# Performance work log

Hardware: AMD Instinct MI355X
Metric: run time of the kernel (lower is better)

Reference implementation:

```python
import jax, jax.numpy as jnp
import numpy as np

CHANNELS = 32
HIDDEN = 1024
LAYERS = 8
NODE_TYPES = 7
N_NODES = 500_000
N_EDGES = 2_000_000
NUM_GRAPHS = 1024


def setup_inputs() -> dict:
    key = jax.random.key(0)
    ks = jax.random.split(key, 8)
    nodes = jax.random.randint(ks[0], (N_NODES,), 0, NODE_TYPES)
    sources = jax.random.randint(ks[1], (N_EDGES,), 0, N_NODES)
    targets = jax.random.randint(ks[2], (N_EDGES,), 0, N_NODES)
    # sorted graph ids covering all NUM_GRAPHS graphs (no empty graphs)
    batch = (jnp.arange(N_NODES) * NUM_GRAPHS) // N_NODES
    emb = jax.random.normal(ks[3], (NODE_TYPES, CHANNELS), dtype=jnp.float32)
    # xavier-normal-ish init for the 8 layers x {out, back} 32x32 convs
    xavier_std = (2.0 / (CHANNELS + CHANNELS)) ** 0.5
    conv_w = jax.random.normal(ks[4], (LAYERS, 2, CHANNELS, CHANNELS), dtype=jnp.float32) * xavier_std
    hidden_w = jax.random.normal(ks[5], (CHANNELS, HIDDEN), dtype=jnp.float32) * 0.05
    hidden_b = jax.random.normal(ks[6], (HIDDEN,), dtype=jnp.float32) * 0.05
    out_w = jax.random.normal(ks[7], (HIDDEN, 1), dtype=jnp.float32) * 0.05
    return dict(nodes=nodes, sources=sources, targets=targets, batch=batch,
                emb=emb, conv_w=conv_w, hidden_w=hidden_w, hidden_b=hidden_b,
                out_w=out_w)


def reference(nodes, sources, targets, batch, emb, conv_w, hidden_w, hidden_b, out_w):
    n = nodes.shape[0]
    ones_e = jnp.ones(sources.shape[0], dtype=jnp.float32)
    # norm = 1 / (1 + in-degree), norm_t = 1 / (1 + out-degree)  [N,1]
    norm = (1.0 / (1.0 + jax.ops.segment_sum(ones_e, targets, num_segments=n)))[:, None]
    norm_t = (1.0 / (1.0 + jax.ops.segment_sum(ones_e, sources, num_segments=n)))[:, None]
    node_counts = jax.ops.segment_sum(jnp.ones(n, dtype=jnp.float32), batch,
                                      num_segments=NUM_GRAPHS)

    x = emb[nodes]  # [N, C]

    def conv(x, s, t, nrm, w):
        # x.index_add(0, t, x[s]) -> x + scatter_add of gathered source feats
        agg = nrm * (x + jax.ops.segment_sum(x[s], t, num_segments=n))
        return jax.nn.relu(agg @ w)

    for l in range(LAYERS):
        x = x + conv(x, sources, targets, norm, conv_w[l, 0]) \
              + conv(x, targets, sources, norm_t, conv_w[l, 1])

    # mean pooling per graph
    g = jax.ops.segment_sum(x, batch, num_segments=NUM_GRAPHS) / node_counts[:, None]
    h = jax.nn.relu(g @ hidden_w + hidden_b)
    return (h @ out_w).squeeze(-1)  # [NUM_GRAPHS]
```

## Files before the change

kernel.cpp:

```cpp
#include <hip/hip_runtime.h>

#define CHANNELS 32
#define HIDDEN 1024
#define LAYERS 8
#define NRANGE 8

typedef __attribute__((ext_vector_type(8))) short short8;
typedef __attribute__((ext_vector_type(4))) float float4v;

__device__ __forceinline__ short f2bf_rne(float f) {
    union { float f; unsigned u; } v; v.f = f;
    unsigned r = v.u + 0x7fffu + ((v.u >> 16) & 1u);
    return (short)(r >> 16);
}
__device__ __forceinline__ float bf2f(short h) {
    union { float f; unsigned u; } v; v.u = ((unsigned)(unsigned short)h) << 16;
    return v.f;
}
__device__ __forceinline__ float bfu2f(unsigned short h) {
    union { float f; unsigned u; } v; v.u = ((unsigned)h) << 16;
    return v.f;
}
__device__ __forceinline__ float bflo(unsigned u) {
    union { float f; unsigned u; } v; v.u = u << 16; return v.f;
}
__device__ __forceinline__ float bfhi(unsigned u) {
    union { float f; unsigned u; } v; v.u = u & 0xffff0000u; return v.f;
}
__device__ __forceinline__ unsigned packbf(float x, float y) {
    return ((unsigned)(unsigned short)f2bf_rne(y) << 16) |
            (unsigned)(unsigned short)f2bf_rne(x);
}


__global__ __launch_bounds__(256)
void pre_kernel(const int* __restrict__ src, const int* __restrict__ tgt,
                int* __restrict__ deg2,
                const int* __restrict__ nodes, const float* __restrict__ emb,
                unsigned short* __restrict__ hi0, unsigned short* __restrict__ lo,
                const int* __restrict__ batch, float* __restrict__ counts,
                int n_nodes, int n_edges, int n_graphs, int rsh,
                int degB, int initB) {
    int bid = blockIdx.x;
    int tid = threadIdx.x;
    if (bid < degB) {
        int r = bid & (NRANGE - 1);
        int chunk = bid >> 3;
        int base = chunk * 2048;
#pragma unroll
        for (int j = 0; j < 8; j++) {
            int e = base + j * 256 + tid;
            if (e < n_edges) {
                int t = __builtin_nontemporal_load(tgt + e);
                int s = __builtin_nontemporal_load(src + e);
                if ((t >> rsh) == r) atomicAdd(&deg2[t], 1);
                if ((s >> rsh) == r) atomicAdd(&deg2[n_nodes + s], 1);
            }
        }
    } else if (bid < degB + initB) {
        int gid = (bid - degB) * 256 + tid;
        int i = gid >> 2, c8 = (gid & 3) * 8;
        if (i < n_nodes) {
            const float* e = emb + nodes[i] * CHANNELS + c8;
            short8 hv, lv;
#pragma unroll
            for (int k = 0; k < 8; k++) {
                float v = e[k];
                short hsh = f2bf_rne(v);
                hv[k] = hsh;
                lv[k] = f2bf_rne(v - bf2f(hsh));
            }
            *(short8*)(hi0 + (size_t)i * CHANNELS + c8) = hv;
            *(short8*)(lo  + (size_t)i * CHANNELS + c8) = lv;
        }
    } else {
        int b = (bid - degB - initB) * 256 + tid;
        if (b < n_graphs) {
            int lo_i = 0, hi_i = n_nodes;
            while (lo_i < hi_i) { int mid = (lo_i + hi_i) >> 1; if (batch[mid] < b) lo_i = mid + 1; else hi_i = mid; }
            int s0 = lo_i;
            lo_i = 0; hi_i = n_nodes;
            while (lo_i < hi_i) { int mid = (lo_i + hi_i) >> 1; if (batch[mid] < b + 1) lo_i = mid + 1; else hi_i = mid; }
            counts[b] = (float)(lo_i - s0);
        }
    }
}


__global__ __launch_bounds__(256)
void scan_pass1(const int* __restrict__ deg, int* __restrict__ bs, int n) {
    __shared__ int sh[256];
    int t = threadIdx.x;
    int base = blockIdx.x * 2048 + t * 8;
    int s = 0;
#pragma unroll
    for (int j = 0; j < 8; j++) { int idx = base + j; if (idx < n) s += deg[idx]; }
    sh[t] = s; __syncthreads();
    for (int st = 128; st > 0; st >>= 1) { if (t < st) sh[t] += sh[t + st]; __syncthreads(); }
    if (t == 0) bs[blockIdx.x] = sh[0];
}

__global__ void scan_pass2(int* __restrict__ bs, int nb) {
    __shared__ int sh[1024];
    int t = threadIdx.x;
    int v = (t < nb) ? bs[t] : 0;
    sh[t] = v; __syncthreads();
    for (int off = 1; off < 1024; off <<= 1) {
        int u = (t >= off) ? sh[t - off] : 0; __syncthreads();
        sh[t] += u; __syncthreads();
    }
    if (t < nb) bs[t] = sh[t] - v;
}

__global__ __launch_bounds__(256)
void scan_pass3(const int* __restrict__ deg, const int* __restrict__ bs,
                int* __restrict__ off, int* __restrict__ cur, int n) {
    __shared__ int sh[256];
    int t = threadIdx.x;
    int base = blockIdx.x * 2048 + t * 8;
    int v[8]; int s = 0;
#pragma unroll
    for (int j = 0; j < 8; j++) { int idx = base + j; v[j] = (idx < n) ? deg[idx] : 0; s += v[j]; }
    sh[t] = s; __syncthreads();
    for (int st = 1; st < 256; st <<= 1) {
        int u = (t >= st) ? sh[t - st] : 0; __syncthreads();
        sh[t] += u; __syncthreads();
    }
    int acc = bs[blockIdx.x] + sh[t] - s;
#pragma unroll
    for (int j = 0; j < 8; j++) {
        int idx = base + j;
        if (idx < n) { off[idx] = acc; cur[idx] = acc; }
        acc += v[j];
    }
}


__global__ __launch_bounds__(256)
void scatter_range_kernel(const int* __restrict__ src, const int* __restrict__ tgt,
                          int* __restrict__ cur2, int* __restrict__ nbr,
                          int n_nodes, int n_edges, int rsh, int rbase) {
    int r = rbase + (blockIdx.x & (NRANGE - 1));
    int chunk = blockIdx.x >> 3;
    int base = chunk * 2048;
#pragma unroll
    for (int j = 0; j < 8; j++) {
        int e = base + j * 256 + threadIdx.x;
        if (e < n_edges) {
            int t = __builtin_nontemporal_load(tgt + e);
            int s = __builtin_nontemporal_load(src + e);
            if ((t >> rsh) == r) { int p = atomicAdd(&cur2[t], 1);           nbr[p] = s; }
            if ((s >> rsh) == r) { int q = atomicAdd(&cur2[n_nodes + s], 1); nbr[q] = t; }
        }
    }
}


__global__ __launch_bounds__(256, 8)
void layer_mfma(const int* __restrict__ off2, const int* __restrict__ nbr,
                const float* __restrict__ wbase,
                const unsigned short* __restrict__ hi_in,
                unsigned short* __restrict__ hi_out,
                unsigned short* __restrict__ lo,
                int n_nodes, int n_edges) {
    __shared__ short A1h[64][32], A2h[64][32];
    __shared__ short W0h[32][32], W1h[32][32];
    __shared__ int offIn[65], offOut[65];

    int tid = threadIdx.x;
    int nodeblock = blockIdx.x * 64;

    for (int idx = tid; idx < CHANNELS * CHANNELS; idx += 256) {
        int k = idx >> 5, n = idx & 31;
        W0h[n][k] = f2bf_rne(wbase[idx]);
        W1h[n][k] = f2bf_rne(wbase[CHANNELS * CHANNELS + idx]);
    }
    if (tid < 65) {
        int idx = nodeblock + tid;
        offIn[tid]  = (idx <= n_nodes) ? off2[idx] : n_edges;
        int idx2 = n_nodes + idx;
        offOut[tid] = (idx2 < 2 * n_nodes) ? off2[idx2] : 2 * n_edges;
    }
    __syncthreads();

    int c = tid & 31, g = tid >> 5;
    int h = c >> 4;
    int cc = c & 15;

    int bi_c, d1_c, bo_c, d2_c, nbl1_c, nbl2_c, node_c;
    float xvx_c, xvy_c;
    {
        int local = g;
        node_c = nodeblock + local;
        bi_c = offIn[local];  d1_c = offIn[local + 1] - bi_c;
        bo_c = offOut[local]; d2_c = offOut[local + 1] - bo_c;
        nbl1_c = (c < d1_c) ? nbr[bi_c + c] : 0;
        nbl2_c = (c < d2_c) ? nbr[bo_c + c] : 0;
        xvx_c = 0.f; xvy_c = 0.f;
        if (node_c < n_nodes) {
            unsigned hp = *(const unsigned*)(hi_in + (size_t)node_c * CHANNELS + 2 * cc);
            unsigned lp = *(const unsigned*)(lo    + (size_t)node_c * CHANNELS + 2 * cc);
            xvx_c = bflo(hp) + bflo(lp);
            xvy_c = bfhi(hp) + bfhi(lp);
        }
    }

    for (int pass = 0; pass < 8; pass++) {
        int bi_n = 0, d1_n = 0, bo_n = 0, d2_n = 0, nbl1_n = 0, nbl2_n = 0, node_n = 0;
        float xvx_n = 0.f, xvy_n = 0.f;
        if (pass < 7) {
            int local = (pass + 1) * 8 + g;
            node_n = nodeblock + local;
            bi_n = offIn[local];  d1_n = offIn[local + 1] - bi_n;
            bo_n = offOut[local]; d2_n = offOut[local + 1] - bo_n;
            nbl1_n = (c < d1_n) ? nbr[bi_n + c] : 0;
            nbl2_n = (c < d2_n) ? nbr[bo_n + c] : 0;
            if (node_n < n_nodes) {
                unsigned hp = *(const unsigned*)(hi_in + (size_t)node_n * CHANNELS + 2 * cc);
                unsigned lp = *(const unsigned*)(lo    + (size_t)node_n * CHANNELS + 2 * cc);
                xvx_n = bflo(hp) + bflo(lp);
                xvy_n = bfhi(hp) + bfhi(lp);
            }
        }

        int local = pass * 8 + g;
        int i = node_c;
        int self = (i < n_nodes) ? i : 0;

        int m1 = d1_c < 32 ? d1_c : 32;
        int m2 = d2_c < 32 ? d2_c : 32;
        int mm = m1 > m2 ? m1 : m2;

        float s1x = 0.f, s1y = 0.f, s2x = 0.f, s2y = 0.f;
        for (int j = 0; j < mm; j += 4) {
            int sl0 = j + h;
            int sl1 = j + 2 + h;
            int p0 = __shfl(nbl1_c, sl0 & 31, 32);
            int p1 = __shfl(nbl1_c, sl1 & 31, 32);
            int q0 = __shfl(nbl2_c, sl0 & 31, 32);
            int q1 = __shfl(nbl2_c, sl1 & 31, 32);
            bool v10 = sl0 < m1, v11 = sl1 < m1;
            bool v20 = sl0 < m2, v21 = sl1 < m2;
            p0 = v10 ? p0 : self;
            p1 = v11 ? p1 : self;
            q0 = v20 ? q0 : self;
            q1 = v21 ? q1 : self;
            unsigned u0 = *(const unsigned*)(hi_in + (size_t)p0 * CHANNELS + 2 * cc);
            unsigned u1 = *(const unsigned*)(hi_in + (size_t)p1 * CHANNELS + 2 * cc);
            unsigned w0 = *(const unsigned*)(hi_in + (size_t)q0 * CHANNELS + 2 * cc);
            unsigned w1 = *(const unsigned*)(hi_in + (size_t)q1 * CHANNELS + 2 * cc);
            s1x += v10 ? bflo(u0) : 0.f;
            s1y += v10 ? bfhi(u0) : 0.f;
            s1x += v11 ? bflo(u1) : 0.f;
            s1y += v11 ? bfhi(u1) : 0.f;
            s2x += v20 ? bflo(w0) : 0.f;
            s2y += v20 ? bfhi(w0) : 0.f;
            s2x += v21 ? bflo(w1) : 0.f;
            s2y += v21 ? bfhi(w1) : 0.f;
        }
        s1x += __shfl_xor(s1x, 16, 32);
        s1y += __shfl_xor(s1y, 16, 32);
        s2x += __shfl_xor(s2x, 16, 32);
        s2y += __shfl_xor(s2y, 16, 32);

        for (int e = bi_c + 32; e < bi_c + d1_c; e++) {
            unsigned u = *(const unsigned*)(hi_in + (size_t)nbr[e] * CHANNELS + 2 * cc);
            s1x += bflo(u); s1y += bfhi(u);
        }
        for (int e = bo_c + 32; e < bo_c + d2_c; e++) {
            unsigned u = *(const unsigned*)(hi_in + (size_t)nbr[e] * CHANNELS + 2 * cc);
            s2x += bflo(u); s2y += bfhi(u);
        }

        unsigned pk1 = 0, pk2 = 0;
        if (i < n_nodes) {
            float n1 = 1.0f / (1.0f + (float)d1_c);
            float n2 = 1.0f / (1.0f + (float)d2_c);
            pk1 = packbf(n1 * (xvx_c + s1x), n1 * (xvy_c + s1y));
            pk2 = packbf(n2 * (xvx_c + s2x), n2 * (xvy_c + s2y));
        }
        unsigned* dst = (h == 0) ? (unsigned*)&A1h[local][2 * cc]
                                 : (unsigned*)&A2h[local][2 * cc];
        *dst = (h == 0) ? pk1 : pk2;

        bi_c = bi_n; d1_c = d1_n; bo_c = bo_n; d2_c = d2_n;
        nbl1_c = nbl1_n; nbl2_c = nbl2_n;
        xvx_c = xvx_n; xvy_c = xvy_n; node_c = node_n;
    }
    __syncthreads();

    int wv = tid >> 6, lane = tid & 63;
    int m = lane & 15, quad = lane >> 4;
    int row0 = wv * 16;

    short8 a1h = *(const short8*)&A1h[row0 + m][quad * 8];
    short8 a2h = *(const short8*)&A2h[row0 + m][quad * 8];

    float4v dd[4];
#pragma unroll
    for (int hh = 0; hh < 2; hh++) {
        int n0 = hh * 16 + m;
        short8 b0h = *(const short8*)&W0h[n0][quad * 8];
        short8 b1h = *(const short8*)&W1h[n0][quad * 8];
        float4v d1 = {0.f, 0.f, 0.f, 0.f};
        d1 = __builtin_amdgcn_mfma_f32_16x16x32_bf16(a1h, b0h, d1, 0, 0, 0);
        float4v d2 = {0.f, 0.f, 0.f, 0.f};
        d2 = __builtin_amdgcn_mfma_f32_16x16x32_bf16(a2h, b1h, d2, 0, 0, 0);
        dd[hh * 2] = d1; dd[hh * 2 + 1] = d2;
    }

#pragma unroll
    for (int hh = 0; hh < 2; hh++) {
        float4v d1 = dd[hh * 2], d2 = dd[hh * 2 + 1];
#pragma unroll
        for (int r = 0; r < 4; r++) {
            int local = row0 + quad * 4 + r;
            int node = nodeblock + local;
            if (node < n_nodes) {
                int col = hh * 16 + m;
                size_t idx = (size_t)node * CHANNELS + col;
                float base = bfu2f(hi_in[idx]) + bfu2f(lo[idx]);
                float v = base + fmaxf(d1[r], 0.f) + fmaxf(d2[r], 0.f);
                short hn = f2bf_rne(v);
                hi_out[idx] = (unsigned short)hn;
                lo[idx]     = (unsigned short)f2bf_rne(v - bf2f(hn));
            }
        }
    }
}


#define POOL_CHUNK 2048

__global__ __launch_bounds__(256)
void pool_kernel(const int* __restrict__ batch,
                 const unsigned short* __restrict__ hi,
                 const unsigned short* __restrict__ lo,
                 float* __restrict__ g, int n_nodes) {
    int c = threadIdx.x & 31;
    int r = threadIdx.x >> 5;
    int base = blockIdx.x * POOL_CHUNK;
    float acc = 0.f;
    int cur = -1;
    for (int it = 0; it < POOL_CHUNK / 8; it++) {
        int node = base + it * 8 + r;
        if (node >= n_nodes) break;
        int b = batch[node];
        if (b != cur) {
            if (cur >= 0) atomicAdd(&g[cur * CHANNELS + c], acc);
            acc = 0.f;
            cur = b;
        }
        size_t idx = (size_t)node * CHANNELS + c;
        acc += bfu2f(hi[idx]) + bfu2f(lo[idx]);
    }
    if (cur >= 0) atomicAdd(&g[cur * CHANNELS + c], acc);
}


__global__ __launch_bounds__(256)
void mlp_kernel(const float* __restrict__ g, const float* __restrict__ counts,
                const float* __restrict__ hidden_w, const float* __restrict__ hidden_b,
                const float* __restrict__ out_w, float* __restrict__ out) {
    __shared__ float grow[CHANNELS];
    __shared__ float red[256];
    int graph = blockIdx.x;
    int tid = threadIdx.x;
    if (tid < CHANNELS) grow[tid] = g[graph * CHANNELS + tid] / counts[graph];
    __syncthreads();
    float partial = 0.f;
    for (int q = 0; q < HIDDEN / 256; q++) {
        int j = q * 256 + tid;
        float h = hidden_b[j];
#pragma unroll
        for (int k = 0; k < CHANNELS; k++) h += grow[k] * hidden_w[k * HIDDEN + j];
        partial += fmaxf(h, 0.f) * out_w[j];
    }
    red[tid] = partial;
    __syncthreads();
    for (int s = 128; s > 0; s >>= 1) {
        if (tid < s) red[tid] += red[tid + s];
        __syncthreads();
    }
    if (tid == 0) out[graph] = red[0];
}


extern "C" void kernel_launch(void* const* d_in, const int* in_sizes, int n_in,
                              void* d_out, int out_size, void* d_ws, size_t ws_size,
                              hipStream_t stream) {
    const int*   nodes    = (const int*)d_in[0];
    const int*   sources  = (const int*)d_in[1];
    const int*   targets  = (const int*)d_in[2];
    const int*   batch    = (const int*)d_in[3];
    const float* emb      = (const float*)d_in[4];
    const float* conv_w   = (const float*)d_in[5];
    const float* hidden_w = (const float*)d_in[6];
    const float* hidden_b = (const float*)d_in[7];
    const float* out_w    = (const float*)d_in[8];
    float* out = (float*)d_out;

    const int n_nodes  = in_sizes[0];
    const int n_edges  = in_sizes[1];
    const int n_graphs = out_size;
    const int n2 = 2 * n_nodes;

    int rsh8 = 0;
    while (((n_nodes - 1) >> rsh8) >= 8) rsh8++;
    int rsh16 = 0;
    while (((n_nodes - 1) >> rsh16) >= 16) rsh16++;

    char* ws = (char*)d_ws;
    unsigned short* hi0 = (unsigned short*)ws; ws += (size_t)n_nodes * CHANNELS * 2;
    unsigned short* hi1 = (unsigned short*)ws; ws += (size_t)n_nodes * CHANNELS * 2;
    unsigned short* lo  = (unsigned short*)ws; ws += (size_t)n_nodes * CHANNELS * 2;
    int*   deg2   = (int*)ws;   ws += (size_t)n2 * 4;
    int*   off2   = (int*)ws;   ws += (size_t)n2 * 4;
    int*   cur2   = (int*)ws;   ws += (size_t)n2 * 4;
    int*   nbr    = (int*)ws;   ws += (size_t)2 * n_edges * 4;
    int*   bsums  = (int*)ws;   ws += 4096;
    float* g      = (float*)ws; ws += (size_t)n_graphs * CHANNELS * 4;
    float* counts = (float*)ws; ws += (size_t)n_graphs * 4;

    hipMemsetAsync(deg2, 0, (size_t)n2 * 4, stream);
    hipMemsetAsync(g, 0, (size_t)n_graphs * CHANNELS * 4, stream);

    int echunks = (n_edges + 2047) / 2048;
    int degB  = echunks * NRANGE;
    int initB = (n_nodes * 4 + 255) / 256;
    int cntB  = (n_graphs + 255) / 256;

    pre_kernel<<<degB + initB + cntB, 256, 0, stream>>>(sources, targets, deg2,
                                                        nodes, emb, hi0, lo,
                                                        batch, counts,
                                                        n_nodes, n_edges, n_graphs,
                                                        rsh8, degB, initB);

    int nblk = (n2 + 2047) / 2048;
    scan_pass1<<<nblk, 256, 0, stream>>>(deg2, bsums, n2);
    scan_pass2<<<1, 1024, 0, stream>>>(bsums, nblk);
    scan_pass3<<<nblk, 256, 0, stream>>>(deg2, bsums, off2, cur2, n2);

    scatter_range_kernel<<<echunks * NRANGE, 256, 0, stream>>>(sources, targets, cur2, nbr,
                                                               n_nodes, n_edges, rsh16, 0);
    scatter_range_kernel<<<echunks * NRANGE, 256, 0, stream>>>(sources, targets, cur2, nbr,
                                                               n_nodes, n_edges, rsh16, 8);

    unsigned short* hin = hi0; unsigned short* hout = hi1;
    int lblocks = (n_nodes + 63) / 64;
    for (int l = 0; l < LAYERS; l++) {
        const float* wbase = conv_w + (size_t)l * 2 * CHANNELS * CHANNELS;
        layer_mfma<<<lblocks, 256, 0, stream>>>(off2, nbr, wbase,
                                                hin, hout, lo, n_nodes, n_edges);
        unsigned short* tmp = hin; hin = hout; hout = tmp;
    }

    int pool_blocks = (n_nodes + POOL_CHUNK - 1) / POOL_CHUNK;
    pool_kernel<<<pool_blocks, 256, 0, stream>>>(batch, hin, lo, g, n_nodes);
    mlp_kernel<<<n_graphs, 256, 0, stream>>>(g, counts, hidden_w, hidden_b, out_w, out);
}
```

Before: 1.486 ms.

## Unroll neighbor gather by eight, use 32-bit indexing, merge scatter launches

The neighbor-gather loop in the layer kernel becomes a macro that issues eight independent loads per step in four guarded blocks, which raises memory-level parallelism. Feature loads switch from size_t pointer arithmetic to 32-bit unsigned indexing. The two 8-range scatter launches are merged into one 16-range launch, and the pool chunk size is halved. The unrolled gather adds registers, which could lower occupancy under launch bounds of 256,8, and merging the scatter launches changes the order of atomic contention.

```diff
diff --git a/kernel.cpp b/kernel.cpp
--- a/kernel.cpp
+++ b/kernel.cpp
@@ -139,9 +139,9 @@
 __global__ __launch_bounds__(256)
 void scatter_range_kernel(const int* __restrict__ src, const int* __restrict__ tgt,
                           int* __restrict__ cur2, int* __restrict__ nbr,
-                          int n_nodes, int n_edges, int rsh, int rbase) {
-    int r = rbase + (blockIdx.x & (NRANGE - 1));
-    int chunk = blockIdx.x >> 3;
+                          int n_nodes, int n_edges, int rsh) {
+    int r = blockIdx.x & 15;
+    int chunk = blockIdx.x >> 4;
     int base = chunk * 2048;
 #pragma unroll
     for (int j = 0; j < 8; j++) {
@@ -169,6 +169,9 @@
 
     int tid = threadIdx.x;
     int nodeblock = blockIdx.x * 64;
+
+    const unsigned* hid = (const unsigned*)hi_in;
+    const unsigned* lod = (const unsigned*)lo;
 
     for (int idx = tid; idx < CHANNELS * CHANNELS; idx += 256) {
         int k = idx >> 5, n = idx & 31;
@@ -198,12 +201,47 @@
         nbl2_c = (c < d2_c) ? nbr[bo_c + c] : 0;
         xvx_c = 0.f; xvy_c = 0.f;
         if (node_c < n_nodes) {
-            unsigned hp = *(const unsigned*)(hi_in + (size_t)node_c * CHANNELS + 2 * cc);
-            unsigned lp = *(const unsigned*)(lo    + (size_t)node_c * CHANNELS + 2 * cc);
+            unsigned hp = hid[(unsigned)(node_c * 16 + cc)];
+            unsigned lp = lod[(unsigned)(node_c * 16 + cc)];
             xvx_c = bflo(hp) + bflo(lp);
             xvy_c = bfhi(hp) + bfhi(lp);
         }
     }
+
+#define GATHER8(B) { \
+    int p0 = __shfl(nbl1_c, (B) + h,     32); \
+    int p1 = __shfl(nbl1_c, (B) + 2 + h, 32); \
+    int p2 = __shfl(nbl1_c, (B) + 4 + h, 32); \
+    int p3 = __shfl(nbl1_c, (B) + 6 + h, 32); \
+    int q0 = __shfl(nbl2_c, (B) + h,     32); \
+    int q1 = __shfl(nbl2_c, (B) + 2 + h, 32); \
+    int q2 = __shfl(nbl2_c, (B) + 4 + h, 32); \
+    int q3 = __shfl(nbl2_c, (B) + 6 + h, 32); \
+    bool a0 = (B) + h     < m1, a1 = (B) + 2 + h < m1; \
+    bool a2 = (B) + 4 + h < m1, a3 = (B) + 6 + h < m1; \
+    bool e0 = (B) + h     < m2, e1 = (B) + 2 + h < m2; \
+    bool e2 = (B) + 4 + h < m2, e3 = (B) + 6 + h < m2; \
+    p0 = a0 ? p0 : self; p1 = a1 ? p1 : self; \
+    p2 = a2 ? p2 : self; p3 = a3 ? p3 : self; \
+    q0 = e0 ? q0 : self; q1 = e1 ? q1 : self; \
+    q2 = e2 ? q2 : self; q3 = e3 ? q3 : self; \
+    unsigned u0 = hid[(unsigned)(p0 * 16 + cc)]; \
+    unsigned u1 = hid[(unsigned)(p1 * 16 + cc)]; \
+    unsigned u2 = hid[(unsigned)(p2 * 16 + cc)]; \
+    unsigned u3 = hid[(unsigned)(p3 * 16 + cc)]; \
+    unsigned w0 = hid[(unsigned)(q0 * 16 + cc)]; \
+    unsigned w1 = hid[(unsigned)(q1 * 16 + cc)]; \
+    unsigned w2 = hid[(unsigned)(q2 * 16 + cc)]; \
+    unsigned w3 = hid[(unsigned)(q3 * 16 + cc)]; \
+    s1x += a0 ? bflo(u0) : 0.f; s1y += a0 ? bfhi(u0) : 0.f; \
+    s1x += a1 ? bflo(u1) : 0.f; s1y += a1 ? bfhi(u1) : 0.f; \
+    s1x += a2 ? bflo(u2) : 0.f; s1y += a2 ? bfhi(u2) : 0.f; \
+    s1x += a3 ? bflo(u3) : 0.f; s1y += a3 ? bfhi(u3) : 0.f; \
+    s2x += e0 ? bflo(w0) : 0.f; s2y += e0 ? bfhi(w0) : 0.f; \
+    s2x += e1 ? bflo(w1) : 0.f; s2y += e1 ? bfhi(w1) : 0.f; \
+    s2x += e2 ? bflo(w2) : 0.f; s2y += e2 ? bfhi(w2) : 0.f; \
+    s2x += e3 ? bflo(w3) : 0.f; s2y += e3 ? bfhi(w3) : 0.f; \
+}
 
     for (int pass = 0; pass < 8; pass++) {
         int bi_n = 0, d1_n = 0, bo_n = 0, d2_n = 0, nbl1_n = 0, nbl2_n = 0, node_n = 0;
@@ -216,8 +254,8 @@
             nbl1_n = (c < d1_n) ? nbr[bi_n + c] : 0;
             nbl2_n = (c < d2_n) ? nbr[bo_n + c] : 0;
             if (node_n < n_nodes) {
-                unsigned hp = *(const unsigned*)(hi_in + (size_t)node_n * CHANNELS + 2 * cc);
-                unsigned lp = *(const unsigned*)(lo    + (size_t)node_n * CHANNELS + 2 * cc);
+                unsigned hp = hid[(unsigned)(node_n * 16 + cc)];
+                unsigned lp = lod[(unsigned)(node_n * 16 + cc)];
                 xvx_n = bflo(hp) + bflo(lp);
                 xvy_n = bfhi(hp) + bfhi(lp);
             }
@@ -232,43 +270,22 @@
         int mm = m1 > m2 ? m1 : m2;
 
         float s1x = 0.f, s1y = 0.f, s2x = 0.f, s2y = 0.f;
-        for (int j = 0; j < mm; j += 4) {
-            int sl0 = j + h;
-            int sl1 = j + 2 + h;
-            int p0 = __shfl(nbl1_c, sl0 & 31, 32);
-            int p1 = __shfl(nbl1_c, sl1 & 31, 32);
-            int q0 = __shfl(nbl2_c, sl0 & 31, 32);
-            int q1 = __shfl(nbl2_c, sl1 & 31, 32);
-            bool v10 = sl0 < m1, v11 = sl1 < m1;
-            bool v20 = sl0 < m2, v21 = sl1 < m2;
-            p0 = v10 ? p0 : self;
-            p1 = v11 ? p1 : self;
-            q0 = v20 ? q0 : self;
-            q1 = v21 ? q1 : self;
-            unsigned u0 = *(const unsigned*)(hi_in + (size_t)p0 * CHANNELS + 2 * cc);
-            unsigned u1 = *(const unsigned*)(hi_in + (size_t)p1 * CHANNELS + 2 * cc);
-            unsigned w0 = *(const unsigned*)(hi_in + (size_t)q0 * CHANNELS + 2 * cc);
-            unsigned w1 = *(const unsigned*)(hi_in + (size_t)q1 * CHANNELS + 2 * cc);
-            s1x += v10 ? bflo(u0) : 0.f;
-            s1y += v10 ? bfhi(u0) : 0.f;
-            s1x += v11 ? bflo(u1) : 0.f;
-            s1y += v11 ? bfhi(u1) : 0.f;
-            s2x += v20 ? bflo(w0) : 0.f;
-            s2y += v20 ? bfhi(w0) : 0.f;
-            s2x += v21 ? bflo(w1) : 0.f;
-            s2y += v21 ? bfhi(w1) : 0.f;
-        }
+        GATHER8(0)
+        if (mm > 8)  GATHER8(8)
+        if (mm > 16) GATHER8(16)
+        if (mm > 24) GATHER8(24)
+
         s1x += __shfl_xor(s1x, 16, 32);
         s1y += __shfl_xor(s1y, 16, 32);
         s2x += __shfl_xor(s2x, 16, 32);
         s2y += __shfl_xor(s2y, 16, 32);
 
         for (int e = bi_c + 32; e < bi_c + d1_c; e++) {
-            unsigned u = *(const unsigned*)(hi_in + (size_t)nbr[e] * CHANNELS + 2 * cc);
+            unsigned u = hid[(unsigned)(nbr[e] * 16 + cc)];
             s1x += bflo(u); s1y += bfhi(u);
         }
         for (int e = bo_c + 32; e < bo_c + d2_c; e++) {
-            unsigned u = *(const unsigned*)(hi_in + (size_t)nbr[e] * CHANNELS + 2 * cc);
+            unsigned u = hid[(unsigned)(nbr[e] * 16 + cc)];
             s2x += bflo(u); s2y += bfhi(u);
         }
 
@@ -287,6 +304,7 @@
         nbl1_c = nbl1_n; nbl2_c = nbl2_n;
         xvx_c = xvx_n; xvy_c = xvy_n; node_c = node_n;
     }
+#undef GATHER8
     __syncthreads();
 
     int wv = tid >> 6, lane = tid & 63;
@@ -330,7 +348,7 @@
 }
 
 
-#define POOL_CHUNK 2048
+#define POOL_CHUNK 1024
 
 __global__ __launch_bounds__(256)
 void pool_kernel(const int* __restrict__ batch,
@@ -441,10 +459,8 @@
     scan_pass2<<<1, 1024, 0, stream>>>(bsums, nblk);
     scan_pass3<<<nblk, 256, 0, stream>>>(deg2, bsums, off2, cur2, n2);
 
-    scatter_range_kernel<<<echunks * NRANGE, 256, 0, stream>>>(sources, targets, cur2, nbr,
-                                                               n_nodes, n_edges, rsh16, 0);
-    scatter_range_kernel<<<echunks * NRANGE, 256, 0, stream>>>(sources, targets, cur2, nbr,
-                                                               n_nodes, n_edges, rsh16, 8);
+    scatter_range_kernel<<<echunks * 16, 256, 0, stream>>>(sources, targets, cur2, nbr,
+                                                           n_nodes, n_edges, rsh16);
 
     unsigned short* hin = hi0; unsigned short* hout = hi1;
     int lblocks = (n_nodes + 63) / 64;
```

New measurement: 1.560 ms. +4.9%, slower.
